# Kernel optimization log

Hardware: AMD Instinct MI355X
Metric: run time of the kernel (lower is better)

## Reference

```python
import jax, jax.numpy as jnp
import numpy as np

F = 128   # flattened observation features
H = 64    # MLP/LSTM hidden size (hardcoded in module)
A = 15    # number of discrete actions
T = 128   # rollout length (timesteps)
B = 2048  # number of parallel envs (batch)


def setup_inputs() -> dict:
    key = jax.random.key(0)
    ks = jax.random.split(key, 12)
    n = lambda k, sh, s=1.0: jax.random.normal(k, sh, jnp.float32) * s
    return {
        "x": n(ks[0], (T * B, F)),
        "done": (jax.random.uniform(ks[1], (T * B,)) < 0.05).astype(jnp.float32),
        "h0": n(ks[2], (1, B, H)),
        "c0": n(ks[3], (1, B, H)),
        # MLP encoder params (Linear stores y = x @ W + b here, W: [in, out])
        "W1": n(ks[4], (F, H), 0.1), "b1": jnp.zeros((H,), jnp.float32),
        "W2": n(ks[5], (H, H), 0.1), "b2": jnp.zeros((H,), jnp.float32),
        # LSTM params, PyTorch layout: weight_ih [4H, H_in], gate order i,f,g,o
        "Wih": n(ks[6], (4 * H, H), 0.1), "bih": jnp.zeros((4 * H,), jnp.float32),
        "Whh": n(ks[7], (4 * H, H), 0.1), "bhh": jnp.zeros((4 * H,), jnp.float32),
        # actor / critic heads
        "Wa": n(ks[8], (H, A), 0.01), "ba": jnp.zeros((A,), jnp.float32),
        "Wc": n(ks[9], (H, 1), 1.0), "bc": jnp.zeros((1,), jnp.float32),
    }


def reference(x, done, h0, c0, W1, b1, W2, b2, Wih, bih, Whh, bhh, Wa, ba, Wc, bc):
    Bsz, Hh = h0.shape[1], h0.shape[2]
    # MLP encoder: Linear -> Tanh -> Linear -> Tanh
    y = jnp.tanh(x @ W1 + b1)
    y = jnp.tanh(y @ W2 + b2)                 # [T*B, H]
    y = y.reshape(-1, Bsz, Hh)                # [T, B, H]
    d = done.reshape(-1, Bsz)                 # [T, B]

    def step(carry, td):
        h, c = carry
        yt, dt = td
        m = (1.0 - dt)[:, None]               # done-mask hidden reset
        h = h * m
        c = c * m
        g = yt @ Wih.T + bih + h @ Whh.T + bhh  # [B, 4H]
        i, f, gg, o = jnp.split(g, 4, axis=-1)
        c = jax.nn.sigmoid(f) * c + jax.nn.sigmoid(i) * jnp.tanh(gg)
        h = jax.nn.sigmoid(o) * jnp.tanh(c)
        return (h, c), h

    (hT, cT), outs = jax.lax.scan(step, (h0[0], c0[0]), (y, d))
    z = outs.reshape(-1, Hh)                  # [T*B, H]
    logits = z @ Wa + ba                      # Categorical logits
    vf = z @ Wc + bc
    return logits, vf, hT[None], cT[None]
```

## Files before the change

kernel.cpp:

```cpp
#include <hip/hip_runtime.h>
#include <hip/hip_bf16.h>
#include <stdint.h>

typedef __bf16  bf16x8 __attribute__((ext_vector_type(8)));
typedef short   s16x8  __attribute__((ext_vector_type(8)));
typedef int     i32x4  __attribute__((ext_vector_type(4)));
typedef float   f32x4  __attribute__((ext_vector_type(4)));

union Frag { s16x8 s; bf16x8 b; i32x4 i; };

static __device__ __forceinline__ short f2bf(float f) {
    union { float f; unsigned u; } v; v.f = f;
    unsigned r = (v.u + 0x7FFFu + ((v.u >> 16) & 1u)) >> 16;
    return (short)r;
}
static __device__ __forceinline__ float bf2f(short s) {
    union { unsigned u; float f; } v; v.u = ((unsigned)(unsigned short)s) << 16;
    return v.f;
}
static __device__ __forceinline__ float fast_rcp(float x) { return __builtin_amdgcn_rcpf(x); }
static __device__ __forceinline__ float sigm(float x) { return fast_rcp(1.0f + __expf(-x)); }
static __device__ __forceinline__ float tanh_fast(float x) {
    float e = __expf(-2.0f * x);
    return (1.0f - e) * fast_rcp(1.0f + e);
}
static __device__ __forceinline__ f32x4 mfma16(bf16x8 a, bf16x8 b, f32x4 c) {
    return __builtin_amdgcn_mfma_f32_16x16x32_bf16(a, b, c, 0, 0, 0);
}

static __device__ __forceinline__ void block_sync_lds() {
    asm volatile("s_waitcnt lgkmcnt(0)\n\ts_barrier" ::: "memory");
}

#define GLDS(gp, lp) __builtin_amdgcn_global_load_lds( \
    (const __attribute__((address_space(1))) void*)(gp), \
    (__attribute__((address_space(3))) void*)(lp), 16, 0, 0)

#define TT 128
#define BB 2048
#define HH 64
#define FF 128
#define AA 15
#define CH 8
#define LOGITS_OFF 0
#define VF_OFF   3932160
#define HT_OFF   4194304
#define CT_OFF   4325376


__global__ __launch_bounds__(256) void enc_kernel(
    const float* __restrict__ x, const float* __restrict__ W1, const float* __restrict__ b1,
    const float* __restrict__ W2, const float* __restrict__ b2, short* __restrict__ y_sw)
{
    __shared__ short w1t[64][136];
    __shared__ short w2t[64][72];
    __shared__ short c1buf[4][16][72];
    __shared__ short ybuf[4][16][72];

    const int tid  = threadIdx.x;
    const int lane = tid & 63;
    const int w    = tid >> 6;
    const int c    = lane & 15;
    const int q    = lane >> 4;

    for (int i = tid; i < 128*64; i += 256) { int k = i >> 6, n = i & 63; w1t[n][k] = f2bf(W1[i]); }
    for (int i = tid; i < 64*64;  i += 256) { int k = i >> 6, n = i & 63; w2t[n][k] = f2bf(W2[i]); }

    float b1v[4], b2v[4];
#pragma unroll
    for (int ct = 0; ct < 4; ++ct) { b1v[ct] = b1[16*ct + c]; b2v[ct] = b2[16*ct + c]; }
    __syncthreads();

    for (int it = 0; it < 4; ++it) {
        const int wt = it*4096 + blockIdx.x*4 + w;
        const int r0 = wt * 16;
        Frag af[4];
#pragma unroll
        for (int kf = 0; kf < 4; ++kf) {
            const float* xp = x + (size_t)(r0 + c)*FF + 32*kf + 8*q;
            f32x4 x0 = *(const f32x4*)xp;
            f32x4 x1 = *(const f32x4*)(xp + 4);
#pragma unroll
            for (int jj = 0; jj < 4; ++jj) { af[kf].s[jj] = f2bf(x0[jj]); af[kf].s[4+jj] = f2bf(x1[jj]); }
        }
        f32x4 acc[4];
#pragma unroll
        for (int ct = 0; ct < 4; ++ct) acc[ct] = (f32x4){b1v[ct], b1v[ct], b1v[ct], b1v[ct]};
#pragma unroll
        for (int kf = 0; kf < 4; ++kf)
#pragma unroll
            for (int ct = 0; ct < 4; ++ct) {
                Frag bf; bf.s = *(const s16x8*)&w1t[16*ct + c][32*kf + 8*q];
                acc[ct] = mfma16(af[kf].b, bf.b, acc[ct]);
            }
#pragma unroll
        for (int ct = 0; ct < 4; ++ct)
#pragma unroll
            for (int i = 0; i < 4; ++i)
                c1buf[w][4*q + i][16*ct + c] = f2bf(tanh_fast(acc[ct][i]));
        Frag a2[2];
#pragma unroll
        for (int kf = 0; kf < 2; ++kf) a2[kf].s = *(const s16x8*)&c1buf[w][c][32*kf + 8*q];
        f32x4 acc2[4];
#pragma unroll
        for (int ct = 0; ct < 4; ++ct) acc2[ct] = (f32x4){b2v[ct], b2v[ct], b2v[ct], b2v[ct]};
#pragma unroll
        for (int kf = 0; kf < 2; ++kf)
#pragma unroll
            for (int ct = 0; ct < 4; ++ct) {
                Frag bf; bf.s = *(const s16x8*)&w2t[16*ct + c][32*kf + 8*q];
                acc2[ct] = mfma16(a2[kf].b, bf.b, acc2[ct]);
            }
#pragma unroll
        for (int ct = 0; ct < 4; ++ct)
#pragma unroll
            for (int i = 0; i < 4; ++i)
                ybuf[w][4*q + i][16*ct + c] = f2bf(tanh_fast(acc2[ct][i]));
#pragma unroll
        for (int kf = 0; kf < 2; ++kf) {
            s16x8 yv = *(const s16x8*)&ybuf[w][c][32*kf + 8*q];
            *(s16x8*)(y_sw + (size_t)wt*1024 + kf*512 + lane*8) = yv;
        }
    }
}

__global__ __launch_bounds__(512, 1) void scan_kernel(
    const short* __restrict__ y_sw, const float* __restrict__ done,
    const float* __restrict__ h0, const float* __restrict__ c0,
    const float* __restrict__ Wih, const float* __restrict__ bih,
    const float* __restrict__ Whh, const float* __restrict__ bhh,
    const float* __restrict__ Wa, const float* __restrict__ ba,
    const float* __restrict__ Wc, const float* __restrict__ bc,
    float* __restrict__ out_logits, float* __restrict__ out_vf,
    float* __restrict__ hT_out, float* __restrict__ cT_out)
{
    __shared__ short ybuf[2][CH][1024];
    __shared__ float gybuf[2][4][4][256];
    __shared__ float obuf[2][CH][16][16];
    __shared__ short zbuf[2][16][72];
    __shared__ short hbuf[2][16][72];
    __shared__ float dbuf[TT+1][16];

    const int tid  = threadIdx.x;
    const int lane = tid & 63;
    const int w    = tid >> 6;
    const int c    = lane & 15;
    const int q    = lane >> 4;
    const int blk  = blockIdx.x;
    const int b0   = blk * 16;
    const bool crit = (w < 4);
    const int hw   = w - 4;

    Frag  wf[4][2];
    float biasv[4];
    Frag  hwf[2];
    float hbv = 0.f;
    float cst[4];

    if (crit) {
        const int jcol = 16*w + c;
#pragma unroll
        for (int a = 0; a < 4; ++a) {
            const int col = 64*a + jcol;
#pragma unroll
            for (int kf = 0; kf < 2; ++kf) {
                const float* wp = Whh + (size_t)col*HH + 32*kf + 8*q;
                f32x4 w0 = *(const f32x4*)wp;
                f32x4 w1 = *(const f32x4*)(wp + 4);
#pragma unroll
                for (int jj = 0; jj < 4; ++jj) { wf[a][kf].s[jj] = f2bf(w0[jj]); wf[a][kf].s[4+jj] = f2bf(w1[jj]); }
            }
        }
    } else {
        const int jcolh = 16*hw + c;
#pragma unroll
        for (int a = 0; a < 4; ++a) {
            const int col = 64*a + jcolh;
            biasv[a] = bih[col] + bhh[col];
#pragma unroll
            for (int kf = 0; kf < 2; ++kf) {
                const float* wp = Wih + (size_t)col*HH + 32*kf + 8*q;
                f32x4 w0 = *(const f32x4*)wp;
                f32x4 w1 = *(const f32x4*)(wp + 4);
#pragma unroll
                for (int jj = 0; jj < 4; ++jj) { wf[a][kf].s[jj] = f2bf(w0[jj]); wf[a][kf].s[4+jj] = f2bf(w1[jj]); }
            }
        }
#pragma unroll
        for (int kf = 0; kf < 2; ++kf)
#pragma unroll
            for (int jj = 0; jj < 8; ++jj) {
                int k = 32*kf + 8*q + jj;
                hwf[kf].s[jj] = f2bf((c < 15) ? Wa[k*AA + c] : Wc[k]);
            }
        hbv = (c < 15) ? ba[c] : bc[0];
#pragma unroll
        for (int i = 0; i < 2; ++i) {
            int j = hw*2 + i;
            const float* gp = done + (size_t)(16*j + (lane >> 2))*BB + b0 + 4*(lane & 3);
            GLDS(gp, &dbuf[16*j][0]);
        }
#pragma unroll
        for (int i = 0; i < 4; ++i) {
            int idx = hw*4 + i, ss = idx >> 1, half = idx & 1;
            const short* gp = y_sw + ((size_t)ss*128 + blk)*1024 + half*512 + lane*8;
            GLDS(gp, &ybuf[0][ss][half*512]);
        }
        __builtin_amdgcn_s_waitcnt(0x0F70);
    }
    if (tid < 16) dbuf[TT][tid] = 0.0f;
    __syncthreads();

    if (crit) {
        const int jcol = 16*w + c;
#pragma unroll
        for (int i = 0; i < 4; ++i) {
            float d0 = dbuf[0][4*q + i];
            float cv = c0[(size_t)(b0 + 4*q + i)*HH + jcol];
            cst[i] = (d0 != 0.0f) ? 0.0f : cv;
        }
        int mm = tid & 15, j4 = (tid >> 4) & 15;
        float dm = dbuf[0][mm];
        f32x4 hv = *(const f32x4*)(h0 + (size_t)(b0 + mm)*HH + 4*j4);
#pragma unroll
        for (int ii = 0; ii < 4; ++ii)
            hbuf[0][mm][4*j4 + ii] = (dm != 0.0f) ? (short)0 : f2bf(hv[ii]);
    } else {
        Frag yc0, yc1;
        yc0.s = *(const s16x8*)&ybuf[0][0][lane*8];
        yc1.s = *(const s16x8*)&ybuf[0][0][512 + lane*8];
#pragma unroll
        for (int a = 0; a < 4; ++a) {
            f32x4 gg = (f32x4){biasv[a], biasv[a], biasv[a], biasv[a]};
            gg = mfma16(yc0.b, wf[a][0].b, gg);
            gg = mfma16(yc1.b, wf[a][1].b, gg);
            *(f32x4*)&gybuf[0][hw][a][lane*4] = gg;
        }
    }
    __syncthreads();

    for (int t = 0; t < TT; ++t) {
        if (crit) {
            const int jcol = 16*w + c;
            const int cur = t & 1;
            Frag hf0, hf1;
            hf0.s = *(const s16x8*)&hbuf[cur][c][8*q];
            hf1.s = *(const s16x8*)&hbuf[cur][c][32 + 8*q];
            f32x4 acc[4];
#pragma unroll
            for (int a = 0; a < 4; ++a) acc[a] = *(const f32x4*)&gybuf[cur][w][a][lane*4];
#pragma unroll
            for (int a = 0; a < 4; ++a) {
                acc[a] = mfma16(hf0.b, wf[a][0].b, acc[a]);
                acc[a] = mfma16(hf1.b, wf[a][1].b, acc[a]);
            }
            const f32x4 dn = *(const f32x4*)&dbuf[t+1][4*q];
#pragma unroll
            for (int i = 0; i < 4; ++i) {
                float gi = acc[0][i], gf = acc[1][i], gg = acc[2][i], go = acc[3][i];
                float cn = sigm(gf)*cst[i] + sigm(gi)*tanh_fast(gg);
                float h  = sigm(go)*tanh_fast(cn);
                short zb = f2bf(h);
                zbuf[cur][4*q + i][jcol] = zb;
                const bool d = (dn[i] != 0.0f);
                cst[i] = d ? 0.0f : cn;
                hbuf[cur ^ 1][4*q + i][jcol] = d ? (short)0 : zb;
            }
        } else {
            if ((t & 7) == 0 && t < 120) {
                const int k = (t >> 3) + 1;
#pragma unroll
                for (int i = 0; i < 4; ++i) {
                    int idx = hw*4 + i, ss = idx >> 1, half = idx & 1;
                    const short* gp = y_sw + ((size_t)(8*k + ss)*128 + blk)*1024 + half*512 + lane*8;
                    GLDS(gp, &ybuf[k & 1][ss][half*512]);
                }
            }
            if ((t & 7) == 1 && t > 8 && w < 6) {
                const int cc = (t >> 3) - 1;
                const int idx = (w - 4)*64 + lane;
                const int s = idx >> 4, r = idx & 15;
                const size_t row = (size_t)(8*cc + s)*BB + b0 + r;
                const float* ob = &obuf[cc & 1][s][r][0];
                float* lp = out_logits + row*AA;
#pragma unroll
                for (int n = 0; n < 15; ++n) lp[n] = ob[n];
                out_vf[row] = ob[15];
            }
            if (t >= 1 && w == 4 + ((t-1) & 3)) {
                const int tp = t - 1;
                Frag zf0, zf1;
                zf0.s = *(const s16x8*)&zbuf[tp & 1][c][8*q];
                zf1.s = *(const s16x8*)&zbuf[tp & 1][c][32 + 8*q];
                f32x4 ha = (f32x4){hbv, hbv, hbv, hbv};
                ha = mfma16(zf0.b, hwf[0].b, ha);
                ha = mfma16(zf1.b, hwf[1].b, ha);
#pragma unroll
                for (int i = 0; i < 4; ++i)
                    obuf[(tp >> 3) & 1][tp & 7][4*q + i][c] = ha[i];
            }
            if (t < TT-1) {
                const int tn = t + 1;
                const int ch = (tn >> 3) & 1, sl = tn & 7;
                Frag yc0, yc1;
                yc0.s = *(const s16x8*)&ybuf[ch][sl][lane*8];
                yc1.s = *(const s16x8*)&ybuf[ch][sl][512 + lane*8];
#pragma unroll
                for (int a = 0; a < 4; ++a) {
                    f32x4 g = (f32x4){biasv[a], biasv[a], biasv[a], biasv[a]};
                    g = mfma16(yc0.b, wf[a][0].b, g);
                    g = mfma16(yc1.b, wf[a][1].b, g);
                    *(f32x4*)&gybuf[tn & 1][hw][a][lane*4] = g;
                }
            }
            if ((t & 7) == 6)
                __builtin_amdgcn_s_waitcnt(0x0F70);
        }
        block_sync_lds();
    }

    if (!crit && w == 7) {
        Frag zf0, zf1;
        zf0.s = *(const s16x8*)&zbuf[1][c][8*q];
        zf1.s = *(const s16x8*)&zbuf[1][c][32 + 8*q];
        f32x4 ha = (f32x4){hbv, hbv, hbv, hbv};
        ha = mfma16(zf0.b, hwf[0].b, ha);
        ha = mfma16(zf1.b, hwf[1].b, ha);
#pragma unroll
        for (int i = 0; i < 4; ++i) obuf[1][7][4*q + i][c] = ha[i];
    }
    __syncthreads();
    if (!crit && w < 6) {
        const int idx = (w - 4)*64 + lane;
        const int s = idx >> 4, r = idx & 15;
        const size_t row = (size_t)(120 + s)*BB + b0 + r;
        const float* ob = &obuf[1][s][r][0];
        float* lp = out_logits + row*AA;
#pragma unroll
        for (int n = 0; n < 15; ++n) lp[n] = ob[n];
        out_vf[row] = ob[15];
    }
    if (crit) {
        const int jcol = 16*w + c;
        int mm = tid & 15, j4 = (tid >> 4) & 15;
        f32x4 hv;
#pragma unroll
        for (int ii = 0; ii < 4; ++ii) hv[ii] = bf2f(zbuf[1][mm][4*j4 + ii]);
        *(f32x4*)(hT_out + (size_t)(b0 + mm)*HH + 4*j4) = hv;
#pragma unroll
        for (int i = 0; i < 4; ++i) cT_out[(size_t)(b0 + 4*q + i)*HH + jcol] = cst[i];
    }
}

extern "C" void kernel_launch(void* const* d_in, const int* in_sizes, int n_in,
                              void* d_out, int out_size, void* d_ws, size_t ws_size,
                              hipStream_t stream) {
    const float* x    = (const float*)d_in[0];
    const float* done = (const float*)d_in[1];
    const float* h0   = (const float*)d_in[2];
    const float* c0   = (const float*)d_in[3];
    const float* W1   = (const float*)d_in[4];
    const float* b1   = (const float*)d_in[5];
    const float* W2   = (const float*)d_in[6];
    const float* b2   = (const float*)d_in[7];
    const float* Wih  = (const float*)d_in[8];
    const float* bih  = (const float*)d_in[9];
    const float* Whh  = (const float*)d_in[10];
    const float* bhh  = (const float*)d_in[11];
    const float* Wa   = (const float*)d_in[12];
    const float* ba   = (const float*)d_in[13];
    const float* Wc   = (const float*)d_in[14];
    const float* bc   = (const float*)d_in[15];
    float* out = (float*)d_out;

    short* y_sw = (short*)d_ws;

    enc_kernel<<<1024, 256, 0, stream>>>(x, W1, b1, W2, b2, y_sw);
    scan_kernel<<<128, 512, 0, stream>>>(y_sw, done, h0, c0, Wih, bih, Whh, bhh,
                                         Wa, ba, Wc, bc,
                                         out + LOGITS_OFF, out + VF_OFF,
                                         out + HT_OFF, out + CT_OFF);
}
```

Baseline: 322.0 us.

## Halve per-block batch to 8 envs and launch 256 scan blocks

The recurrent scan kernel now processes 8 environments per block instead of 16, doubling the grid to 256 blocks so more of the MI355X's compute units run the latency-bound sequential loop. The encoder writes y in a matching 8-row layout, and the MFMA 16-row tiles are half-filled, with lanes redistributed via ds_bpermute so each lane handles 2 rows of the elementwise LSTM update. The gate nonlinearities are also fused to share reciprocals. The cost is wasted MFMA work on padded rows and extra permute instructions on each step of the critical path.

Result: faster. 310.2 us (-3.7%).

```diff
diff --git a/kernel.cpp b/kernel.cpp
--- a/kernel.cpp
+++ b/kernel.cpp
@@ -116,10 +116,15 @@
 #pragma unroll
             for (int i = 0; i < 4; ++i)
                 ybuf[w][4*q + i][16*ct + c] = f2bf(tanh_fast(acc2[ct][i]));
-#pragma unroll
-        for (int kf = 0; kf < 2; ++kf) {
-            s16x8 yv = *(const s16x8*)&ybuf[w][c][32*kf + 8*q];
-            *(s16x8*)(y_sw + (size_t)wt*1024 + kf*512 + lane*8) = yv;
+        {
+            const int kf2 = lane >> 5;
+            const int c8  = (lane >> 2) & 7;
+            const int qq  = lane & 3;
+#pragma unroll
+            for (int g = 0; g < 2; ++g) {
+                s16x8 yv = *(const s16x8*)&ybuf[w][c8 + 8*g][32*kf2 + 8*qq];
+                *(s16x8*)(y_sw + ((size_t)(wt >> 7)*256 + (size_t)(wt & 127)*2 + g)*512 + lane*8) = yv;
+            }
         }
     }
 }
@@ -134,12 +139,12 @@
     float* __restrict__ out_logits, float* __restrict__ out_vf,
     float* __restrict__ hT_out, float* __restrict__ cT_out)
 {
-    __shared__ short ybuf[2][CH][1024];
-    __shared__ float gybuf[2][4][4][256];
-    __shared__ float obuf[2][CH][16][16];
-    __shared__ short zbuf[2][16][72];
-    __shared__ short hbuf[2][16][72];
-    __shared__ float dbuf[TT+1][16];
+    __shared__ short ybuf[2][CH][512];
+    __shared__ float gybuf[2][4][4][128];
+    __shared__ float obuf[2][CH][8][16];
+    __shared__ short zbuf[2][8][72];
+    __shared__ short hbuf[2][8][72];
+    __shared__ float dbuf[TT+1][8];
 
     const int tid  = threadIdx.x;
     const int lane = tid & 63;
@@ -147,15 +152,16 @@
     const int c    = lane & 15;
     const int q    = lane >> 4;
     const int blk  = blockIdx.x;
-    const int b0   = blk * 16;
+    const int b0   = blk * 8;
     const bool crit = (w < 4);
     const int hw   = w - 4;
+    const int r0   = 4*(q & 1) + 2*(q >> 1);
 
     Frag  wf[4][2];
     float biasv[4];
     Frag  hwf[2];
     float hbv = 0.f;
-    float cst[4];
+    float cst0 = 0.f, cst1 = 0.f;
 
     if (crit) {
         const int jcol = 16*w + c;
@@ -194,47 +200,50 @@
                 hwf[kf].s[jj] = f2bf((c < 15) ? Wa[k*AA + c] : Wc[k]);
             }
         hbv = (c < 15) ? ba[c] : bc[0];
+        {
+            const int t0 = hw * 32;
+            const float* gp = done + (size_t)(t0 + (lane >> 1))*BB + b0 + 4*(lane & 1);
+            GLDS(gp, &dbuf[t0][0]);
+        }
 #pragma unroll
         for (int i = 0; i < 2; ++i) {
-            int j = hw*2 + i;
-            const float* gp = done + (size_t)(16*j + (lane >> 2))*BB + b0 + 4*(lane & 3);
-            GLDS(gp, &dbuf[16*j][0]);
-        }
-#pragma unroll
-        for (int i = 0; i < 4; ++i) {
-            int idx = hw*4 + i, ss = idx >> 1, half = idx & 1;
-            const short* gp = y_sw + ((size_t)ss*128 + blk)*1024 + half*512 + lane*8;
-            GLDS(gp, &ybuf[0][ss][half*512]);
+            const int ss = hw*2 + i;
+            const short* gp = y_sw + ((size_t)ss*256 + blk)*512 + lane*8;
+            GLDS(gp, &ybuf[0][ss][0]);
         }
         __builtin_amdgcn_s_waitcnt(0x0F70);
     }
-    if (tid < 16) dbuf[TT][tid] = 0.0f;
+    if (tid < 8) dbuf[TT][tid] = 0.0f;
     __syncthreads();
 
     if (crit) {
         const int jcol = 16*w + c;
-#pragma unroll
-        for (int i = 0; i < 4; ++i) {
-            float d0 = dbuf[0][4*q + i];
-            float cv = c0[(size_t)(b0 + 4*q + i)*HH + jcol];
-            cst[i] = (d0 != 0.0f) ? 0.0f : cv;
-        }
-        int mm = tid & 15, j4 = (tid >> 4) & 15;
-        float dm = dbuf[0][mm];
-        f32x4 hv = *(const f32x4*)(h0 + (size_t)(b0 + mm)*HH + 4*j4);
-#pragma unroll
-        for (int ii = 0; ii < 4; ++ii)
-            hbuf[0][mm][4*j4 + ii] = (dm != 0.0f) ? (short)0 : f2bf(hv[ii]);
+        {
+            float d0 = dbuf[0][r0 + 0];
+            float d1 = dbuf[0][r0 + 1];
+            float cv0 = c0[(size_t)(b0 + r0 + 0)*HH + jcol];
+            float cv1 = c0[(size_t)(b0 + r0 + 1)*HH + jcol];
+            cst0 = (d0 != 0.0f) ? 0.0f : cv0;
+            cst1 = (d1 != 0.0f) ? 0.0f : cv1;
+        }
+        if (tid < 128) {
+            int mm = tid & 7, j4 = (tid >> 3) & 15;
+            float dm = dbuf[0][mm];
+            f32x4 hv = *(const f32x4*)(h0 + (size_t)(b0 + mm)*HH + 4*j4);
+#pragma unroll
+            for (int ii = 0; ii < 4; ++ii)
+                hbuf[0][mm][4*j4 + ii] = (dm != 0.0f) ? (short)0 : f2bf(hv[ii]);
+        }
     } else {
         Frag yc0, yc1;
-        yc0.s = *(const s16x8*)&ybuf[0][0][lane*8];
-        yc1.s = *(const s16x8*)&ybuf[0][0][512 + lane*8];
+        yc0.s = *(const s16x8*)&ybuf[0][0][((c & 7)*4 + q)*8];
+        yc1.s = *(const s16x8*)&ybuf[0][0][(32 + (c & 7)*4 + q)*8];
 #pragma unroll
         for (int a = 0; a < 4; ++a) {
             f32x4 gg = (f32x4){biasv[a], biasv[a], biasv[a], biasv[a]};
             gg = mfma16(yc0.b, wf[a][0].b, gg);
             gg = mfma16(yc1.b, wf[a][1].b, gg);
-            *(f32x4*)&gybuf[0][hw][a][lane*4] = gg;
+            if (lane < 32) *(f32x4*)&gybuf[0][hw][a][lane*4] = gg;
         }
     }
     __syncthreads();
@@ -244,42 +253,56 @@
             const int jcol = 16*w + c;
             const int cur = t & 1;
             Frag hf0, hf1;
-            hf0.s = *(const s16x8*)&hbuf[cur][c][8*q];
-            hf1.s = *(const s16x8*)&hbuf[cur][c][32 + 8*q];
+            hf0.s = *(const s16x8*)&hbuf[cur][c & 7][8*q];
+            hf1.s = *(const s16x8*)&hbuf[cur][c & 7][32 + 8*q];
             f32x4 acc[4];
 #pragma unroll
-            for (int a = 0; a < 4; ++a) acc[a] = *(const f32x4*)&gybuf[cur][w][a][lane*4];
+            for (int a = 0; a < 4; ++a) acc[a] = *(const f32x4*)&gybuf[cur][w][a][(lane & 31)*4];
 #pragma unroll
             for (int a = 0; a < 4; ++a) {
                 acc[a] = mfma16(hf0.b, wf[a][0].b, acc[a]);
                 acc[a] = mfma16(hf1.b, wf[a][1].b, acc[a]);
             }
-            const f32x4 dn = *(const f32x4*)&dbuf[t+1][4*q];
-#pragma unroll
-            for (int i = 0; i < 4; ++i) {
-                float gi = acc[0][i], gf = acc[1][i], gg = acc[2][i], go = acc[3][i];
-                float cn = sigm(gf)*cst[i] + sigm(gi)*tanh_fast(gg);
-                float h  = sigm(go)*tanh_fast(cn);
-                short zb = f2bf(h);
-                zbuf[cur][4*q + i][jcol] = zb;
-                const bool d = (dn[i] != 0.0f);
-                cst[i] = d ? 0.0f : cn;
-                hbuf[cur ^ 1][4*q + i][jcol] = d ? (short)0 : zb;
-            }
+            const int pidx = (lane ^ 32) << 2;
+            float g0[4], g1[4];
+            const bool hiq = (q >= 2);
+#pragma unroll
+            for (int a = 0; a < 4; ++a) {
+                float s0 = __int_as_float(__builtin_amdgcn_ds_bpermute(pidx, __float_as_int(acc[a][2])));
+                float s1 = __int_as_float(__builtin_amdgcn_ds_bpermute(pidx, __float_as_int(acc[a][3])));
+                g0[a] = hiq ? s0 : acc[a][0];
+                g1[a] = hiq ? s1 : acc[a][1];
+            }
+            const float dn0 = dbuf[t+1][r0 + 0];
+            const float dn1 = dbuf[t+1][r0 + 1];
+#define ELEM(GV, CSTV, RI, DN) {                                        \
+            float ei = __expf(-GV[0]), ef = __expf(-GV[1]);             \
+            float eg = __expf(-2.0f*GV[2]), eo = __expf(-GV[3]);        \
+            float term = (1.0f - eg) * fast_rcp((1.0f + ei)*(1.0f + eg)); \
+            float cn = fast_rcp(1.0f + ef)*CSTV + term;                 \
+            float ec = __expf(-2.0f*cn);                                \
+            float hv = (1.0f - ec) * fast_rcp((1.0f + eo)*(1.0f + ec)); \
+            short zb = f2bf(hv);                                        \
+            zbuf[cur][RI][jcol] = zb;                                   \
+            const bool d = ((DN) != 0.0f);                              \
+            CSTV = d ? 0.0f : cn;                                       \
+            hbuf[cur ^ 1][RI][jcol] = d ? (short)0 : zb; }
+            ELEM(g0, cst0, r0 + 0, dn0)
+            ELEM(g1, cst1, r0 + 1, dn1)
+#undef ELEM
         } else {
             if ((t & 7) == 0 && t < 120) {
                 const int k = (t >> 3) + 1;
 #pragma unroll
-                for (int i = 0; i < 4; ++i) {
-                    int idx = hw*4 + i, ss = idx >> 1, half = idx & 1;
-                    const short* gp = y_sw + ((size_t)(8*k + ss)*128 + blk)*1024 + half*512 + lane*8;
-                    GLDS(gp, &ybuf[k & 1][ss][half*512]);
+                for (int i = 0; i < 2; ++i) {
+                    const int ss = hw*2 + i;
+                    const short* gp = y_sw + ((size_t)(8*k + ss)*256 + blk)*512 + lane*8;
+                    GLDS(gp, &ybuf[k & 1][ss][0]);
                 }
             }
-            if ((t & 7) == 1 && t > 8 && w < 6) {
+            if ((t & 7) == 1 && t > 8 && w == 4) {
                 const int cc = (t >> 3) - 1;
-                const int idx = (w - 4)*64 + lane;
-                const int s = idx >> 4, r = idx & 15;
+                const int s = lane >> 3, r = lane & 7;
                 const size_t row = (size_t)(8*cc + s)*BB + b0 + r;
                 const float* ob = &obuf[cc & 1][s][r][0];
                 float* lp = out_logits + row*AA;
@@ -287,30 +310,32 @@
                 for (int n = 0; n < 15; ++n) lp[n] = ob[n];
                 out_vf[row] = ob[15];
             }
-            if (t >= 1 && w == 4 + ((t-1) & 3)) {
+            if (t >= 1 && w == 4 + ((t + 2) & 3)) {
                 const int tp = t - 1;
                 Frag zf0, zf1;
-                zf0.s = *(const s16x8*)&zbuf[tp & 1][c][8*q];
-                zf1.s = *(const s16x8*)&zbuf[tp & 1][c][32 + 8*q];
+                zf0.s = *(const s16x8*)&zbuf[tp & 1][c & 7][8*q];
+                zf1.s = *(const s16x8*)&zbuf[tp & 1][c & 7][32 + 8*q];
                 f32x4 ha = (f32x4){hbv, hbv, hbv, hbv};
                 ha = mfma16(zf0.b, hwf[0].b, ha);
                 ha = mfma16(zf1.b, hwf[1].b, ha);
-#pragma unroll
-                for (int i = 0; i < 4; ++i)
-                    obuf[(tp >> 3) & 1][tp & 7][4*q + i][c] = ha[i];
+                if (q < 2) {
+#pragma unroll
+                    for (int i = 0; i < 4; ++i)
+                        obuf[(tp >> 3) & 1][tp & 7][4*q + i][c] = ha[i];
+                }
             }
             if (t < TT-1) {
                 const int tn = t + 1;
                 const int ch = (tn >> 3) & 1, sl = tn & 7;
                 Frag yc0, yc1;
-                yc0.s = *(const s16x8*)&ybuf[ch][sl][lane*8];
-                yc1.s = *(const s16x8*)&ybuf[ch][sl][512 + lane*8];
+                yc0.s = *(const s16x8*)&ybuf[ch][sl][((c & 7)*4 + q)*8];
+                yc1.s = *(const s16x8*)&ybuf[ch][sl][(32 + (c & 7)*4 + q)*8];
 #pragma unroll
                 for (int a = 0; a < 4; ++a) {
                     f32x4 g = (f32x4){biasv[a], biasv[a], biasv[a], biasv[a]};
                     g = mfma16(yc0.b, wf[a][0].b, g);
                     g = mfma16(yc1.b, wf[a][1].b, g);
-                    *(f32x4*)&gybuf[tn & 1][hw][a][lane*4] = g;
+                    if (lane < 32) *(f32x4*)&gybuf[tn & 1][hw][a][lane*4] = g;
                 }
             }
             if ((t & 7) == 6)
@@ -321,18 +346,19 @@
 
     if (!crit && w == 7) {
         Frag zf0, zf1;
-        zf0.s = *(const s16x8*)&zbuf[1][c][8*q];
-        zf1.s = *(const s16x8*)&zbuf[1][c][32 + 8*q];
+        zf0.s = *(const s16x8*)&zbuf[1][c & 7][8*q];
+        zf1.s = *(const s16x8*)&zbuf[1][c & 7][32 + 8*q];
         f32x4 ha = (f32x4){hbv, hbv, hbv, hbv};
         ha = mfma16(zf0.b, hwf[0].b, ha);
         ha = mfma16(zf1.b, hwf[1].b, ha);
-#pragma unroll
-        for (int i = 0; i < 4; ++i) obuf[1][7][4*q + i][c] = ha[i];
+        if (q < 2) {
+#pragma unroll
+            for (int i = 0; i < 4; ++i) obuf[1][7][4*q + i][c] = ha[i];
+        }
     }
     __syncthreads();
-    if (!crit && w < 6) {
-        const int idx = (w - 4)*64 + lane;
-        const int s = idx >> 4, r = idx & 15;
+    if (!crit && w == 4) {
+        const int s = lane >> 3, r = lane & 7;
         const size_t row = (size_t)(120 + s)*BB + b0 + r;
         const float* ob = &obuf[1][s][r][0];
         float* lp = out_logits + row*AA;
@@ -340,15 +366,17 @@
         for (int n = 0; n < 15; ++n) lp[n] = ob[n];
         out_vf[row] = ob[15];
     }
+    if (tid < 128) {
+        int mm = tid & 7, j4 = (tid >> 3) & 15;
+        f32x4 hv;
+#pragma unroll
+        for (int ii = 0; ii < 4; ++ii) hv[ii] = bf2f(zbuf[1][mm][4*j4 + ii]);
+        *(f32x4*)(hT_out + (size_t)(b0 + mm)*HH + 4*j4) = hv;
+    }
     if (crit) {
         const int jcol = 16*w + c;
-        int mm = tid & 15, j4 = (tid >> 4) & 15;
-        f32x4 hv;
-#pragma unroll
-        for (int ii = 0; ii < 4; ++ii) hv[ii] = bf2f(zbuf[1][mm][4*j4 + ii]);
-        *(f32x4*)(hT_out + (size_t)(b0 + mm)*HH + 4*j4) = hv;
-#pragma unroll
-        for (int i = 0; i < 4; ++i) cT_out[(size_t)(b0 + 4*q + i)*HH + jcol] = cst[i];
+        cT_out[(size_t)(b0 + r0 + 0)*HH + jcol] = cst0;
+        cT_out[(size_t)(b0 + r0 + 1)*HH + jcol] = cst1;
     }
 }
 
@@ -376,7 +404,7 @@
     short* y_sw = (short*)d_ws;
 
     enc_kernel<<<1024, 256, 0, stream>>>(x, W1, b1, W2, b2, y_sw);
-    scan_kernel<<<128, 512, 0, stream>>>(y_sw, done, h0, c0, Wih, bih, Whh, bhh,
+    scan_kernel<<<256, 512, 0, stream>>>(y_sw, done, h0, c0, Wih, bih, Whh, bhh,
                                          Wa, ba, Wc, bc,
                                          out + LOGITS_OFF, out + VF_OFF,
                                          out + HT_OFF, out + CT_OFF);
```
